# Kernel tuning notes

Hardware: AMD Instinct MI355X
Metric: run time of the kernel (lower is better)

## Reference

```python
import jax, jax.numpy as jnp
import numpy as np

B, N, C = 2, 2048, 1536
H = 8
D = C // H  # 192, must match M's size


def setup_inputs() -> dict:
    key = jax.random.key(0)
    ks = jax.random.split(key, 5)
    x = jax.random.normal(ks[0], (B, N, C), dtype=jnp.float32)
    # nn.Linear(dim, 3*dim, bias=False): weight shape (3C, C)
    W_qkv = jax.random.normal(ks[1], (3 * C, C), dtype=jnp.float32) * (C ** -0.5)
    # nn.Linear(dim, dim) with bias
    W_proj = jax.random.normal(ks[2], (C, C), dtype=jnp.float32) * (C ** -0.5)
    b_proj = jnp.zeros((C,), dtype=jnp.float32)
    scale = jnp.asarray(D ** -0.5, dtype=jnp.float32)  # learned scalar, init head_dim**-0.5
    M = jnp.eye(D, dtype=jnp.float32)  # learned Mahalanobis metric, init identity
    return {"x": x, "W_qkv": W_qkv, "W_proj": W_proj, "b_proj": b_proj,
            "scale": scale, "M": M}


def reference(x, W_qkv, W_proj, b_proj, scale, M):
    Bv, Nv, Cv = x.shape
    qkv = x @ W_qkv.T                                  # [B,N,3C]
    qkv = qkv.reshape(Bv, Nv, 3, H, D).transpose(2, 0, 3, 1, 4)  # [3,B,H,N,D]
    q, k, v = qkv[0], qkv[1], qkv[2]
    q_M = q @ M                                        # [B,H,N,D]
    k_M = k @ M                                        # [B,H,N,D]
    qMq = jnp.sum(q * q_M, axis=-1, keepdims=True)     # [B,H,N,1]
    kMk = jnp.sum(k * k_M, axis=-1, keepdims=True)     # [B,H,N,1]
    kMk = jnp.swapaxes(kMk, -2, -1)                    # [B,H,1,N]
    qMk = jnp.einsum('bhnd,bhmd->bhnm', q_M, k)        # [B,H,N,N]
    dists = qMq + kMk - 2.0 * qMk                      # Mahalanobis quadratic form
    attn = jax.nn.softmax(-dists * scale, axis=-1)     # [B,H,N,N]
    out = jnp.einsum('bhnm,bhmd->bhnd', attn, v)       # [B,H,N,D]
    out = jnp.swapaxes(out, 1, 2).reshape(Bv, Nv, Cv)  # [B,N,C]
    out = out @ W_proj.T + b_proj
    return (out, attn, M)
```

## Files before the change

kernel.cpp:

```cpp
#include <hip/hip_runtime.h>

typedef _Float16 f16;
typedef __attribute__((ext_vector_type(8))) _Float16 f16x8;
typedef __attribute__((ext_vector_type(4))) float f32x4;

#define LOG2E 1.4426950408889634f
#define MFMA16(a, b, c) __builtin_amdgcn_mfma_f32_16x16x32_f16((a), (b), (c), 0, 0, 0)


__device__ __forceinline__ void gl16(const void* g, void* l) {
    __builtin_amdgcn_global_load_lds(
        (const __attribute__((address_space(1))) unsigned int*)g,
        (__attribute__((address_space(3))) unsigned int*)l, 16, 0, 0);
}

__global__ void k_cvt(const float* __restrict__ src, f16* __restrict__ dst, int n4) {
    int i = blockIdx.x * blockDim.x + threadIdx.x;
    if (i >= n4) return;
    float4 v = ((const float4*)src)[i];
    union { f16 h[4]; short4 s4; } u;
    u.h[0] = (f16)v.x; u.h[1] = (f16)v.y; u.h[2] = (f16)v.z; u.h[3] = (f16)v.w;
    ((short4*)dst)[i] = u.s4;
}

__global__ void k_cvtM(const float* __restrict__ M, f16* __restrict__ Mt) {
    int i = blockIdx.x * 256 + threadIdx.x;
    if (i >= 192 * 192) return;
    int d = i / 192, e = i - (i / 192) * 192;
    Mt[d * 192 + e] = (f16)M[e * 192 + d];
}

__global__ __launch_bounds__(256) void k_gemm_qkv(
    const f16* __restrict__ A, const f16* __restrict__ Bw,
    f16* __restrict__ Qh, f16* __restrict__ Kh, f16* __restrict__ Vp)
{
    __shared__ __align__(16) char S[32768];
    const int tid = threadIdx.x, lane = tid & 63, w = tid >> 6;
    const int bid = blockIdx.x;
    const int xcd = bid & 7, cc = bid >> 3;
    const int mb = xcd * 4 + cc / 36, nb = cc - (cc / 36) * 36;
    const int m0 = mb * 128, n0 = nb * 128;
    const int sec = nb >= 24 ? 2 : (nb >= 12 ? 1 : 0);
    const int wm = (w & 1) * 64, wn = (w >> 1) * 64;
    const int L = lane & 15, g = lane >> 4;
    const char* Ab = (const char*)A;
    const char* Bb = (const char*)Bw;

    const char* gA[2]; const char* gB[2]; int ldso[2];
#pragma unroll
    for (int q = 0; q < 2; ++q) {
        int s = w * 128 + q * 64 + lane;
        int swz = ((s & 3) ^ ((s >> 2) & 3)) * 16;
        gA[q] = Ab + (size_t)(m0 + (s >> 2)) * 3072 + swz;
        gB[q] = Bb + (size_t)(n0 + (s >> 2)) * 3072 + swz;
        ldso[q] = w * 2048 + q * 1024;
    }
    const int gx = ((g ^ (L & 3)) << 4);

    f32x4 acc[4][4] = {};
#pragma unroll
    for (int q = 0; q < 2; ++q) {
        gl16(gA[q], S + ldso[q]);
        gl16(gB[q], S + 8192 + ldso[q]);
    }
    int buf = 0;
    for (int kk = 0; kk < 48; ++kk) {
        __syncthreads();
        if (kk < 47) {
            int nb_ = (buf ^ 1) * 16384;
#pragma unroll
            for (int q = 0; q < 2; ++q) {
                gl16(gA[q] + (kk + 1) * 64, S + nb_ + ldso[q]);
                gl16(gB[q] + (kk + 1) * 64, S + nb_ + 8192 + ldso[q]);
            }
        }
        const char* AsB = S + buf * 16384;
        const char* BsB = AsB + 8192;
        f16x8 af[4], bf[4];
#pragma unroll
        for (int i = 0; i < 4; ++i) {
            af[i] = *(const f16x8*)(AsB + (wm + i * 16 + L) * 64 + gx);
            bf[i] = *(const f16x8*)(BsB + (wn + i * 16 + L) * 64 + gx);
        }
        if (sec < 2) {
#pragma unroll
            for (int i = 0; i < 4; ++i)
#pragma unroll
                for (int j = 0; j < 4; ++j)
                    acc[i][j] = MFMA16(bf[j], af[i], acc[i][j]);
        } else {
#pragma unroll
            for (int i = 0; i < 4; ++i)
#pragma unroll
                for (int j = 0; j < 4; ++j)
                    acc[i][j] = MFMA16(af[i], bf[j], acc[i][j]);
        }
        buf ^= 1;
    }

    if (sec == 2) {
#pragma unroll
        for (int i = 0; i < 4; ++i)
#pragma unroll
            for (int j = 0; j < 4; ++j) {
                int rem = n0 + wn + j * 16 + L - 3072;
                int h = rem / 192, d = rem - h * 192;
                int gm = m0 + wm + i * 16 + g * 4;
                int gb = gm >> 11, nn = gm & 2047;
                union { f16 h4[4]; short4 s4; } u;
#pragma unroll
                for (int r = 0; r < 4; ++r) u.h4[r] = (f16)acc[i][j][r];
                int nnp = (nn & ~31) | (((nn >> 2) & 3) << 3) | (((nn >> 4) & 1) << 2) | (nn & 3);
                *(short4*)(Vp + (size_t)((gb * 8 + h) * 192 + d) * 2048 + nnp) = u.s4;
            }
    } else {
        f16* base = sec == 0 ? Qh : Kh;
#pragma unroll
        for (int i = 0; i < 4; ++i) {
            int gm = m0 + wm + i * 16 + L;
            int gb = gm >> 11, nn = gm & 2047;
#pragma unroll
            for (int j = 0; j < 4; ++j) {
                int rem = n0 + wn + j * 16 + g * 4 - sec * 1536;
                int h = rem / 192, d = rem - h * 192;
                union { f16 h4[4]; short4 s4; } u;
#pragma unroll
                for (int r = 0; r < 4; ++r) u.h4[r] = (f16)acc[i][j][r];
                *(short4*)(base + (size_t)((gb * 8 + h) * 2048 + nn) * 192 + d) = u.s4;
            }
        }
    }
}

__global__ __launch_bounds__(256) void k_mgemm(
    const f16* __restrict__ Qh, const f16* __restrict__ Kh,
    const f16* __restrict__ Mt, f16* __restrict__ QMh,
    const float* __restrict__ scale_p, float* __restrict__ qmq, float* __restrict__ kmk)
{
    const int tid = threadIdx.x, lane = tid & 63, w = tid >> 6;
    const int L = lane & 15, g = lane >> 4;
    const int isK = blockIdx.y;
    const f16* src = isK ? Kh : Qh;
    float* rowdot = isK ? kmk : qmq;
    const int row0 = blockIdx.x * 64 + w * 16;
    const int tokrow = row0 + L;
    f16x8 af[6];
#pragma unroll
    for (int ks = 0; ks < 6; ++ks)
        af[ks] = *(const f16x8*)((const char*)src + (size_t)tokrow * 384 + ks * 64 + g * 16);
    f32x4 acc[12] = {};
#pragma unroll
    for (int ct = 0; ct < 12; ++ct)
#pragma unroll
        for (int ks = 0; ks < 6; ++ks) {
            f16x8 bf = *(const f16x8*)((const char*)Mt + (ct * 16 + L) * 384 + ks * 64 + g * 16);
            acc[ct] = MFMA16(bf, af[ks], acc[ct]);
        }
    if (!isK) {
#pragma unroll
        for (int ct = 0; ct < 12; ++ct) {
            union { f16 h4[4]; short4 s4; } u;
#pragma unroll
            for (int r = 0; r < 4; ++r) u.h4[r] = (f16)acc[ct][r];
            *(short4*)(QMh + (size_t)tokrow * 192 + ct * 16 + g * 4) = u.s4;
        }
    }
    float s = 0.f;
#pragma unroll
    for (int ct = 0; ct < 12; ++ct) {
        union { short4 s4; f16 h[4]; } kv;
        kv.s4 = *(const short4*)(src + (size_t)tokrow * 192 + ct * 16 + g * 4);
#pragma unroll
        for (int r = 0; r < 4; ++r) s += acc[ct][r] * (float)kv.h[r];
    }
    s += __shfl_xor(s, 16); s += __shfl_xor(s, 32);
    if (lane < 16) rowdot[row0 + lane] = s * scale_p[0] * LOG2E;
}

__global__ __launch_bounds__(256) void k_attn(
    const f16* __restrict__ QMh, const f16* __restrict__ Kh,
    const f16* __restrict__ Vp, const float* __restrict__ kmk,
    const float* __restrict__ qmq, const float* __restrict__ scale_p,
    float* __restrict__ attn, f16* __restrict__ ctx, float* __restrict__ lrow)
{
    __shared__ __align__(16) char KsB[2][12288];
    __shared__ __align__(16) char VsB[2][15360];
    const int tid = threadIdx.x, lane = tid & 63, w = tid >> 6;
    const int L = lane & 15, g = lane >> 4;
    const int bx = blockIdx.x;
    const int bh = (bx & 7) * 2 + (bx >> 8);
    const int qb = (bx >> 3) & 31;
    const int row0 = qb * 64 + w * 16;
    const float a2 = 2.f * scale_p[0] * LOG2E;

    const char* qbase = (const char*)QMh + (size_t)(bh * 2048 + row0) * 384;
    f16x8 qf[6];
#pragma unroll
    for (int ks = 0; ks < 6; ++ks)
        qf[ks] = *(const f16x8*)(qbase + L * 384 + ks * 64 + g * 16);
    const char* Kb = (const char*)Kh + (size_t)bh * 2048 * 384;
    const char* Vb = (const char*)Vp + (size_t)bh * 192 * 4096;
    const float* kmkrow = kmk + bh * 2048;
    const float Crow = qmq[bh * 2048 + row0 + L];

    int ksrc[3], kdst[3], vsrc[3], vdst[3];
#pragma unroll
    for (int i = 0; i < 3; ++i) {
        int s = tid + 256 * i;
        int r = s / 24, c16 = s - r * 24;
        ksrc[i] = r * 384 + c16 * 16;
        kdst[i] = r * 384 + (((c16 & ~7) | ((c16 & 7) ^ (r & 7))) << 4);
        vsrc[i] = (s >> 2) * 4096 + (s & 3) * 16;
        vdst[i] = (s >> 2) * 80 + (s & 3) * 16;
    }
    int kslot[6];
#pragma unroll
    for (int ks = 0; ks < 6; ++ks) {
        int slot = ks * 4 + g;
        kslot[ks] = (((slot & ~7) | ((slot & 7) ^ (L & 7))) << 4);
    }

    int4 stk[3], stv[3];
#pragma unroll
    for (int i = 0; i < 3; ++i) {
        stk[i] = *(const int4*)(Kb + ksrc[i]);
        stv[i] = *(const int4*)(Vb + vsrc[i]);
    }
    f32x4 cacc[12] = {};
    float lacc = 0.f;
    float m_run = -3.0e38f, sc = 0.f;
    float* arow = attn + (size_t)(bh * 2048 + row0 + L) * 2048;

    for (int c = 0; c < 64; ++c) {
        char* Kl = KsB[c & 1];
        char* Vl = VsB[c & 1];
#pragma unroll
        for (int i = 0; i < 3; ++i) {
            *(int4*)(Kl + kdst[i]) = stk[i];
            *(int4*)(Vl + vdst[i]) = stv[i];
        }
        if (c < 63) {
#pragma unroll
            for (int i = 0; i < 3; ++i) {
                stk[i] = *(const int4*)(Kb + (size_t)(c + 1) * 12288 + ksrc[i]);
                stv[i] = *(const int4*)(Vb + (size_t)(c + 1) * 64 + vsrc[i]);
            }
        }
        __syncthreads();
        f32x4 a0 = {}, a1 = {};
#pragma unroll
        for (int ks = 0; ks < 6; ++ks) {
            f16x8 kf0 = *(const f16x8*)(Kl + L * 384 + kslot[ks]);
            f16x8 kf1 = *(const f16x8*)(Kl + (16 + L) * 384 + kslot[ks]);
            a0 = MFMA16(kf0, qf[ks], a0);
            a1 = MFMA16(kf1, qf[ks], a1);
        }
        float4 km0 = *(const float4*)(kmkrow + c * 32 + g * 4);
        float4 km1 = *(const float4*)(kmkrow + c * 32 + 16 + g * 4);
        float e8[8];
        e8[0] = a2 * a0[0] - km0.x - Crow;
        e8[1] = a2 * a0[1] - km0.y - Crow;
        e8[2] = a2 * a0[2] - km0.z - Crow;
        e8[3] = a2 * a0[3] - km0.w - Crow;
        e8[4] = a2 * a1[0] - km1.x - Crow;
        e8[5] = a2 * a1[1] - km1.y - Crow;
        e8[6] = a2 * a1[2] - km1.z - Crow;
        e8[7] = a2 * a1[3] - km1.w - Crow;
        float mx = fmaxf(fmaxf(fmaxf(e8[0], e8[1]), fmaxf(e8[2], e8[3])),
                         fmaxf(fmaxf(e8[4], e8[5]), fmaxf(e8[6], e8[7])));
        mx = fmaxf(mx, __shfl_xor(mx, 16));
        mx = fmaxf(mx, __shfl_xor(mx, 32));
        if (__any(mx > m_run + 4.f)) {
            float mnew = fmaxf(m_run, mx);
            float fr = __builtin_amdgcn_exp2f(m_run - mnew);
            lacc *= fr;
            float frc[4];
#pragma unroll
            for (int r = 0; r < 4; ++r) frc[r] = __shfl(fr, g * 4 + r);
#pragma unroll
            for (int dt = 0; dt < 12; ++dt)
#pragma unroll
                for (int r = 0; r < 4; ++r) cacc[dt][r] *= frc[r];
            m_run = mnew;
            sc = __builtin_amdgcn_exp2f(-m_run);
        }
        float p[8], ps[8];
#pragma unroll
        for (int j = 0; j < 8; ++j) {
            p[j] = __builtin_amdgcn_exp2f(e8[j]);
            ps[j] = p[j] * sc;
        }
        *(float4*)(arow + c * 32 + g * 4)      = make_float4(p[0], p[1], p[2], p[3]);
        *(float4*)(arow + c * 32 + 16 + g * 4) = make_float4(p[4], p[5], p[6], p[7]);
        lacc += ((ps[0] + ps[1]) + (ps[2] + ps[3])) + ((ps[4] + ps[5]) + (ps[6] + ps[7]));
        f16x8 pa;
        pa[0] = (f16)ps[0]; pa[1] = (f16)ps[1]; pa[2] = (f16)ps[2]; pa[3] = (f16)ps[3];
        pa[4] = (f16)ps[4]; pa[5] = (f16)ps[5]; pa[6] = (f16)ps[6]; pa[7] = (f16)ps[7];
#pragma unroll
        for (int dt = 0; dt < 12; ++dt) {
            f16x8 vf = *(const f16x8*)(Vl + (dt * 16 + L) * 80 + g * 16);
            cacc[dt] = MFMA16(pa, vf, cacc[dt]);
        }
    }
    lacc += __shfl_xor(lacc, 16);
    lacc += __shfl_xor(lacc, 32);
    if (g == 0) lrow[bh * 2048 + row0 + L] = __builtin_amdgcn_exp2f(-m_run) / lacc;
    float linv_r[4];
#pragma unroll
    for (int r = 0; r < 4; ++r) linv_r[r] = 1.f / __shfl(lacc, g * 4 + r);

    __syncthreads();
    char* scr = (char*)KsB + w * 6144;
#pragma unroll
    for (int dt = 0; dt < 12; ++dt)
#pragma unroll
        for (int r = 0; r < 4; ++r)
            *(f16*)(scr + (g * 4 + r) * 384 + (dt * 16 + L) * 2)
                = (f16)(cacc[dt][r] * linv_r[r]);
    const int b = bh >> 3, h = bh & 7;
#pragma unroll
    for (int t = 0; t < 6; ++t) {
        int chunk = t * 64 + lane;
        int tok = chunk / 24, c16 = chunk - tok * 24;
        int4 v = *(const int4*)(scr + tok * 384 + c16 * 16);
        *(int4*)((char*)ctx + ((size_t)(b * 2048 + row0 + tok) * 1536 + h * 192) * 2 + c16 * 16) = v;
    }
}

__global__ __launch_bounds__(256) void k_norm(float* __restrict__ attn,
                                              const float* __restrict__ lrow)
{
    const int row = blockIdx.x * 8 + (threadIdx.x >> 5);
    const int t = threadIdx.x & 31;
    const float f = lrow[row];
    float4* p = (float4*)(attn + (size_t)row * 2048) + t;
#pragma unroll
    for (int i = 0; i < 16; ++i) {
        float4 v = p[(size_t)i * 32];
        v.x *= f; v.y *= f; v.z *= f; v.w *= f;
        p[(size_t)i * 32] = v;
    }
}

__global__ __launch_bounds__(256) void k_proj(
    const f16* __restrict__ A, const f16* __restrict__ Bw,
    const float* __restrict__ bias, float* __restrict__ out)
{
    __shared__ __align__(16) char S[32768];
    const int tid = threadIdx.x, lane = tid & 63, w = tid >> 6;
    const int bid = blockIdx.x;
    const int xcd = bid & 7, cc = bid >> 3;
    const int mb = xcd * 4 + cc / 12, nbk = cc - (cc / 12) * 12;
    const int m0 = mb * 128, n0 = nbk * 128;
    const int wm = (w & 1) * 64, wn = (w >> 1) * 64;
    const int L = lane & 15, g = lane >> 4;
    const char* Ab = (const char*)A;
    const char* Bb = (const char*)Bw;

    const char* gA[2]; const char* gB[2]; int ldso[2];
#pragma unroll
    for (int q = 0; q < 2; ++q) {
        int s = w * 128 + q * 64 + lane;
        int swz = ((s & 3) ^ ((s >> 2) & 3)) * 16;
        gA[q] = Ab + (size_t)(m0 + (s >> 2)) * 3072 + swz;
        gB[q] = Bb + (size_t)(n0 + (s >> 2)) * 3072 + swz;
        ldso[q] = w * 2048 + q * 1024;
    }
    const int gx = ((g ^ (L & 3)) << 4);

    f32x4 acc[4][4] = {};
#pragma unroll
    for (int q = 0; q < 2; ++q) {
        gl16(gA[q], S + ldso[q]);
        gl16(gB[q], S + 8192 + ldso[q]);
    }
    int buf = 0;
    for (int kk = 0; kk < 48; ++kk) {
        __syncthreads();
        if (kk < 47) {
            int nb_ = (buf ^ 1) * 16384;
#pragma unroll
            for (int q = 0; q < 2; ++q) {
                gl16(gA[q] + (kk + 1) * 64, S + nb_ + ldso[q]);
                gl16(gB[q] + (kk + 1) * 64, S + nb_ + 8192 + ldso[q]);
            }
        }
        const char* AsB = S + buf * 16384;
        const char* BsB = AsB + 8192;
        f16x8 af[4], bf[4];
#pragma unroll
        for (int i = 0; i < 4; ++i) {
            af[i] = *(const f16x8*)(AsB + (wm + i * 16 + L) * 64 + gx);
            bf[i] = *(const f16x8*)(BsB + (wn + i * 16 + L) * 64 + gx);
        }
#pragma unroll
        for (int i = 0; i < 4; ++i)
#pragma unroll
            for (int j = 0; j < 4; ++j)
                acc[i][j] = MFMA16(bf[j], af[i], acc[i][j]);
        buf ^= 1;
    }
#pragma unroll
    for (int i = 0; i < 4; ++i) {
        int token = m0 + wm + i * 16 + L;
#pragma unroll
        for (int j = 0; j < 4; ++j) {
            int gnb = n0 + wn + j * 16 + g * 4;
            float4 bv = *(const float4*)(bias + gnb);
            float4 v = make_float4(acc[i][j][0] + bv.x, acc[i][j][1] + bv.y,
                                   acc[i][j][2] + bv.z, acc[i][j][3] + bv.w);
            *(float4*)(out + (size_t)token * 1536 + gnb) = v;
        }
    }
}

extern "C" void kernel_launch(void* const* d_in, const int* in_sizes, int n_in,
                              void* d_out, int out_size, void* d_ws, size_t ws_size,
                              hipStream_t stream)
{
    const float* x     = (const float*)d_in[0];
    const float* Wqkv  = (const float*)d_in[1];
    const float* Wproj = (const float*)d_in[2];
    const float* bproj = (const float*)d_in[3];
    const float* scale = (const float*)d_in[4];
    const float* M     = (const float*)d_in[5];
    float* out  = (float*)d_out;
    float* attn = out + 6291456;

    char* p = (char*)d_ws;
    f16* x_h     = (f16*)p;  p += 12582912;
    f16* Wqkv_h  = (f16*)p;  p += 14155776;
    f16* Wproj_h = (f16*)p;  p += 4718592;
    f16* Mt_h    = (f16*)p;  p += 73728;
    f16* Qh      = (f16*)p;  p += 12582912;
    f16* Kh      = (f16*)p;  p += 12582912;
    f16* Vp      = (f16*)p;  p += 12582912;
    f16* QMh     = (f16*)p;  p += 12582912;
    float* qmq   = (float*)p; p += 131072;
    float* kmk   = (float*)p; p += 131072;
    float* lrow  = (float*)p; p += 131072;
    f16* ctx     = (f16*)p;  p += 12582912;

    k_cvt<<<6144, 256, 0, stream>>>(x, x_h, 1572864);
    k_cvt<<<6912, 256, 0, stream>>>(Wqkv, Wqkv_h, 1769472);
    k_cvt<<<2304, 256, 0, stream>>>(Wproj, Wproj_h, 589824);
    k_cvtM<<<144, 256, 0, stream>>>(M, Mt_h);
    k_gemm_qkv<<<1152, 256, 0, stream>>>(x_h, Wqkv_h, Qh, Kh, Vp);
    k_mgemm<<<dim3(512, 2), 256, 0, stream>>>(Qh, Kh, Mt_h, QMh, scale, qmq, kmk);
    k_attn<<<512, 256, 0, stream>>>(QMh, Kh, Vp, kmk, qmq, scale, attn, ctx, lrow);
    k_norm<<<4096, 256, 0, stream>>>(attn, lrow);
    k_proj<<<384, 256, 0, stream>>>(ctx, Wproj_h, bproj, out);
    hipMemcpyAsync(out + 73400320, M, 36864 * 4, hipMemcpyDeviceToDevice, stream);
}
```

Before: 447.8 us.

## Precompute softmax row stats, split attention over key halves, drop normalize pass

Adds a stats kernel that computes the row max and log-sum per query row with a QK-only pass. The attention kernel then writes already-normalized probabilities directly, so the separate read-modify-write normalization of the attention matrix is gone. Attention is split into two key halves to double the block count, with fp32 partial outputs summed by a new combine kernel. The three fp32-to-fp16 conversion launches are merged into one. In exchange, QK^T is recomputed, a large fp32 partial buffer is written and read, and the V tile is single-buffered behind an extra barrier.

```diff
diff --git a/kernel.cpp b/kernel.cpp
--- a/kernel.cpp
+++ b/kernel.cpp
@@ -14,13 +14,18 @@
         (__attribute__((address_space(3))) unsigned int*)l, 16, 0, 0);
 }
 
-__global__ void k_cvt(const float* __restrict__ src, f16* __restrict__ dst, int n4) {
-    int i = blockIdx.x * blockDim.x + threadIdx.x;
-    if (i >= n4) return;
-    float4 v = ((const float4*)src)[i];
+__global__ void k_cvt_all(const float* __restrict__ x, const float* __restrict__ wq,
+                          const float* __restrict__ wp, f16* __restrict__ xh,
+                          f16* __restrict__ wqh, f16* __restrict__ wph) {
+    int i = blockIdx.x * 256 + threadIdx.x;
+    const float4* s; short4* d; int off;
+    if (i < 1572864) { s = (const float4*)x; d = (short4*)xh; off = i; }
+    else if (i < 3342336) { s = (const float4*)wq; d = (short4*)wqh; off = i - 1572864; }
+    else { s = (const float4*)wp; d = (short4*)wph; off = i - 3342336; }
+    float4 v = s[off];
     union { f16 h[4]; short4 s4; } u;
     u.h[0] = (f16)v.x; u.h[1] = (f16)v.y; u.h[2] = (f16)v.z; u.h[3] = (f16)v.w;
-    ((short4*)dst)[i] = u.s4;
+    d[off] = u.s4;
 }
 
 __global__ void k_cvtM(const float* __restrict__ M, f16* __restrict__ Mt) {
@@ -177,14 +182,12 @@
     if (lane < 16) rowdot[row0 + lane] = s * scale_p[0] * LOG2E;
 }
 
-__global__ __launch_bounds__(256) void k_attn(
+__global__ __launch_bounds__(256) void k_stats(
     const f16* __restrict__ QMh, const f16* __restrict__ Kh,
-    const f16* __restrict__ Vp, const float* __restrict__ kmk,
-    const float* __restrict__ qmq, const float* __restrict__ scale_p,
-    float* __restrict__ attn, f16* __restrict__ ctx, float* __restrict__ lrow)
+    const float* __restrict__ kmk, const float* __restrict__ qmq,
+    const float* __restrict__ scale_p, float* __restrict__ moff)
 {
     __shared__ __align__(16) char KsB[2][12288];
-    __shared__ __align__(16) char VsB[2][15360];
     const int tid = threadIdx.x, lane = tid & 63, w = tid >> 6;
     const int L = lane & 15, g = lane >> 4;
     const int bx = blockIdx.x;
@@ -199,19 +202,16 @@
     for (int ks = 0; ks < 6; ++ks)
         qf[ks] = *(const f16x8*)(qbase + L * 384 + ks * 64 + g * 16);
     const char* Kb = (const char*)Kh + (size_t)bh * 2048 * 384;
-    const char* Vb = (const char*)Vp + (size_t)bh * 192 * 4096;
     const float* kmkrow = kmk + bh * 2048;
     const float Crow = qmq[bh * 2048 + row0 + L];
 
-    int ksrc[3], kdst[3], vsrc[3], vdst[3];
+    int ksrc[3], kdst[3];
 #pragma unroll
     for (int i = 0; i < 3; ++i) {
         int s = tid + 256 * i;
         int r = s / 24, c16 = s - r * 24;
         ksrc[i] = r * 384 + c16 * 16;
         kdst[i] = r * 384 + (((c16 & ~7) | ((c16 & 7) ^ (r & 7))) << 4);
-        vsrc[i] = (s >> 2) * 4096 + (s & 3) * 16;
-        vdst[i] = (s >> 2) * 80 + (s & 3) * 16;
     }
     int kslot[6];
 #pragma unroll
@@ -219,32 +219,19 @@
         int slot = ks * 4 + g;
         kslot[ks] = (((slot & ~7) | ((slot & 7) ^ (L & 7))) << 4);
     }
-
-    int4 stk[3], stv[3];
-#pragma unroll
-    for (int i = 0; i < 3; ++i) {
-        stk[i] = *(const int4*)(Kb + ksrc[i]);
-        stv[i] = *(const int4*)(Vb + vsrc[i]);
-    }
-    f32x4 cacc[12] = {};
-    float lacc = 0.f;
-    float m_run = -3.0e38f, sc = 0.f;
-    float* arow = attn + (size_t)(bh * 2048 + row0 + L) * 2048;
-
+    int4 stk[3];
+#pragma unroll
+    for (int i = 0; i < 3; ++i) stk[i] = *(const int4*)(Kb + ksrc[i]);
+
+    float m_run = -3.0e38f, l_run = 0.f;
     for (int c = 0; c < 64; ++c) {
         char* Kl = KsB[c & 1];
-        char* Vl = VsB[c & 1];
-#pragma unroll
-        for (int i = 0; i < 3; ++i) {
-            *(int4*)(Kl + kdst[i]) = stk[i];
-            *(int4*)(Vl + vdst[i]) = stv[i];
-        }
+#pragma unroll
+        for (int i = 0; i < 3; ++i) *(int4*)(Kl + kdst[i]) = stk[i];
         if (c < 63) {
 #pragma unroll
-            for (int i = 0; i < 3; ++i) {
+            for (int i = 0; i < 3; ++i)
                 stk[i] = *(const int4*)(Kb + (size_t)(c + 1) * 12288 + ksrc[i]);
-                stv[i] = *(const int4*)(Vb + (size_t)(c + 1) * 64 + vsrc[i]);
-            }
         }
         __syncthreads();
         f32x4 a0 = {}, a1 = {};
@@ -270,76 +257,146 @@
                          fmaxf(fmaxf(e8[4], e8[5]), fmaxf(e8[6], e8[7])));
         mx = fmaxf(mx, __shfl_xor(mx, 16));
         mx = fmaxf(mx, __shfl_xor(mx, 32));
-        if (__any(mx > m_run + 4.f)) {
-            float mnew = fmaxf(m_run, mx);
-            float fr = __builtin_amdgcn_exp2f(m_run - mnew);
-            lacc *= fr;
-            float frc[4];
-#pragma unroll
-            for (int r = 0; r < 4; ++r) frc[r] = __shfl(fr, g * 4 + r);
-#pragma unroll
-            for (int dt = 0; dt < 12; ++dt)
-#pragma unroll
-                for (int r = 0; r < 4; ++r) cacc[dt][r] *= frc[r];
-            m_run = mnew;
-            sc = __builtin_amdgcn_exp2f(-m_run);
-        }
-        float p[8], ps[8];
-#pragma unroll
-        for (int j = 0; j < 8; ++j) {
-            p[j] = __builtin_amdgcn_exp2f(e8[j]);
-            ps[j] = p[j] * sc;
-        }
+        float mn = fmaxf(m_run, mx);
+        float sum = 0.f;
+#pragma unroll
+        for (int j = 0; j < 8; ++j) sum += __builtin_amdgcn_exp2f(e8[j] - mn);
+        l_run = l_run * __builtin_amdgcn_exp2f(m_run - mn) + sum;
+        m_run = mn;
+    }
+    l_run += __shfl_xor(l_run, 16);
+    l_run += __shfl_xor(l_run, 32);
+    if (g == 0) moff[bh * 2048 + row0 + L] = m_run + __log2f(l_run);
+}
+
+__global__ __launch_bounds__(256, 4) void k_attn(
+    const f16* __restrict__ QMh, const f16* __restrict__ Kh,
+    const f16* __restrict__ Vp, const float* __restrict__ kmk,
+    const float* __restrict__ qmq, const float* __restrict__ scale_p,
+    const float* __restrict__ moff,
+    float* __restrict__ attn, float* __restrict__ pacc)
+{
+    __shared__ __align__(16) char KsB[2][12288];
+    __shared__ __align__(16) char VsB[15360];
+    const int tid = threadIdx.x, lane = tid & 63, w = tid >> 6;
+    const int L = lane & 15, g = lane >> 4;
+    const int bx = blockIdx.x;
+    const int xcd = bx & 7, cc = bx >> 3;
+    const int bh = xcd * 2 + (cc >> 6);
+    const int qb = (cc >> 1) & 31;
+    const int kh = cc & 1;
+    const int c0 = kh * 32;
+    const int row0 = qb * 64 + w * 16;
+    const float a2 = 2.f * scale_p[0] * LOG2E;
+
+    const char* qbase = (const char*)QMh + (size_t)(bh * 2048 + row0) * 384;
+    f16x8 qf[6];
+#pragma unroll
+    for (int ks = 0; ks < 6; ++ks)
+        qf[ks] = *(const f16x8*)(qbase + L * 384 + ks * 64 + g * 16);
+    const char* Kb = (const char*)Kh + (size_t)bh * 2048 * 384;
+    const char* Vb = (const char*)Vp + (size_t)bh * 192 * 4096;
+    const float* kmkrow = kmk + bh * 2048;
+    const float Crow = qmq[bh * 2048 + row0 + L];
+    const float mo = moff[bh * 2048 + row0 + L];
+
+    int ksrc[3], kdst[3], vsrc[3], vdst[3];
+#pragma unroll
+    for (int i = 0; i < 3; ++i) {
+        int s = tid + 256 * i;
+        int r = s / 24, c16 = s - r * 24;
+        ksrc[i] = r * 384 + c16 * 16;
+        kdst[i] = r * 384 + (((c16 & ~7) | ((c16 & 7) ^ (r & 7))) << 4);
+        vsrc[i] = (s >> 2) * 4096 + (s & 3) * 16;
+        vdst[i] = (s >> 2) * 80 + (s & 3) * 16;
+    }
+    int kslot[6];
+#pragma unroll
+    for (int ks = 0; ks < 6; ++ks) {
+        int slot = ks * 4 + g;
+        kslot[ks] = (((slot & ~7) | ((slot & 7) ^ (L & 7))) << 4);
+    }
+
+    int4 stk[3], stv[3];
+#pragma unroll
+    for (int i = 0; i < 3; ++i) {
+        stk[i] = *(const int4*)(Kb + (size_t)c0 * 12288 + ksrc[i]);
+        stv[i] = *(const int4*)(Vb + (size_t)c0 * 64 + vsrc[i]);
+    }
+    f32x4 cacc[12] = {};
+    float* arow = attn + (size_t)(bh * 2048 + row0 + L) * 2048;
+
+    for (int cl = 0; cl < 32; ++cl) {
+        const int c = c0 + cl;
+        char* Kl = KsB[cl & 1];
+#pragma unroll
+        for (int i = 0; i < 3; ++i) *(int4*)(Kl + kdst[i]) = stk[i];
+        __syncthreads();
+#pragma unroll
+        for (int i = 0; i < 3; ++i) *(int4*)(VsB + vdst[i]) = stv[i];
+        __syncthreads();
+        if (cl < 31) {
+#pragma unroll
+            for (int i = 0; i < 3; ++i) {
+                stk[i] = *(const int4*)(Kb + (size_t)(c + 1) * 12288 + ksrc[i]);
+                stv[i] = *(const int4*)(Vb + (size_t)(c + 1) * 64 + vsrc[i]);
+            }
+        }
+        f32x4 a0 = {}, a1 = {};
+#pragma unroll
+        for (int ks = 0; ks < 6; ++ks) {
+            f16x8 kf0 = *(const f16x8*)(Kl + L * 384 + kslot[ks]);
+            f16x8 kf1 = *(const f16x8*)(Kl + (16 + L) * 384 + kslot[ks]);
+            a0 = MFMA16(kf0, qf[ks], a0);
+            a1 = MFMA16(kf1, qf[ks], a1);
+        }
+        float4 km0 = *(const float4*)(kmkrow + c * 32 + g * 4);
+        float4 km1 = *(const float4*)(kmkrow + c * 32 + 16 + g * 4);
+        float p[8];
+        p[0] = __builtin_amdgcn_exp2f(a2 * a0[0] - km0.x - Crow - mo);
+        p[1] = __builtin_amdgcn_exp2f(a2 * a0[1] - km0.y - Crow - mo);
+        p[2] = __builtin_amdgcn_exp2f(a2 * a0[2] - km0.z - Crow - mo);
+        p[3] = __builtin_amdgcn_exp2f(a2 * a0[3] - km0.w - Crow - mo);
+        p[4] = __builtin_amdgcn_exp2f(a2 * a1[0] - km1.x - Crow - mo);
+        p[5] = __builtin_amdgcn_exp2f(a2 * a1[1] - km1.y - Crow - mo);
+        p[6] = __builtin_amdgcn_exp2f(a2 * a1[2] - km1.z - Crow - mo);
+        p[7] = __builtin_amdgcn_exp2f(a2 * a1[3] - km1.w - Crow - mo);
         *(float4*)(arow + c * 32 + g * 4)      = make_float4(p[0], p[1], p[2], p[3]);
         *(float4*)(arow + c * 32 + 16 + g * 4) = make_float4(p[4], p[5], p[6], p[7]);
-        lacc += ((ps[0] + ps[1]) + (ps[2] + ps[3])) + ((ps[4] + ps[5]) + (ps[6] + ps[7]));
         f16x8 pa;
-        pa[0] = (f16)ps[0]; pa[1] = (f16)ps[1]; pa[2] = (f16)ps[2]; pa[3] = (f16)ps[3];
-        pa[4] = (f16)ps[4]; pa[5] = (f16)ps[5]; pa[6] = (f16)ps[6]; pa[7] = (f16)ps[7];
+        pa[0] = (f16)p[0]; pa[1] = (f16)p[1]; pa[2] = (f16)p[2]; pa[3] = (f16)p[3];
+        pa[4] = (f16)p[4]; pa[5] = (f16)p[5]; pa[6] = (f16)p[6]; pa[7] = (f16)p[7];
 #pragma unroll
         for (int dt = 0; dt < 12; ++dt) {
-            f16x8 vf = *(const f16x8*)(Vl + (dt * 16 + L) * 80 + g * 16);
+            f16x8 vf = *(const f16x8*)(VsB + (dt * 16 + L) * 80 + g * 16);
             cacc[dt] = MFMA16(pa, vf, cacc[dt]);
         }
     }
-    lacc += __shfl_xor(lacc, 16);
-    lacc += __shfl_xor(lacc, 32);
-    if (g == 0) lrow[bh * 2048 + row0 + L] = __builtin_amdgcn_exp2f(-m_run) / lacc;
-    float linv_r[4];
-#pragma unroll
-    for (int r = 0; r < 4; ++r) linv_r[r] = 1.f / __shfl(lacc, g * 4 + r);
-
-    __syncthreads();
-    char* scr = (char*)KsB + w * 6144;
 #pragma unroll
     for (int dt = 0; dt < 12; ++dt)
 #pragma unroll
         for (int r = 0; r < 4; ++r)
-            *(f16*)(scr + (g * 4 + r) * 384 + (dt * 16 + L) * 2)
-                = (f16)(cacc[dt][r] * linv_r[r]);
-    const int b = bh >> 3, h = bh & 7;
-#pragma unroll
-    for (int t = 0; t < 6; ++t) {
-        int chunk = t * 64 + lane;
-        int tok = chunk / 24, c16 = chunk - tok * 24;
-        int4 v = *(const int4*)(scr + tok * 384 + c16 * 16);
-        *(int4*)((char*)ctx + ((size_t)(b * 2048 + row0 + tok) * 1536 + h * 192) * 2 + c16 * 16) = v;
-    }
-}
-
-__global__ __launch_bounds__(256) void k_norm(float* __restrict__ attn,
-                                              const float* __restrict__ lrow)
-{
-    const int row = blockIdx.x * 8 + (threadIdx.x >> 5);
-    const int t = threadIdx.x & 31;
-    const float f = lrow[row];
-    float4* p = (float4*)(attn + (size_t)row * 2048) + t;
-#pragma unroll
-    for (int i = 0; i < 16; ++i) {
-        float4 v = p[(size_t)i * 32];
-        v.x *= f; v.y *= f; v.z *= f; v.w *= f;
-        p[(size_t)i * 32] = v;
-    }
+            pacc[((size_t)kh * 32768 + bh * 2048 + row0 + g * 4 + r) * 192 + dt * 16 + L]
+                = cacc[dt][r];
+}
+
+__global__ __launch_bounds__(256) void k_comb(const float* __restrict__ pacc,
+                                              f16* __restrict__ ctx)
+{
+    int idx = blockIdx.x * 256 + threadIdx.x;
+    int row = idx / 24;
+    int d = (idx - row * 24) * 8;
+    const float* p0 = pacc + (size_t)row * 192 + d;
+    const float* p1 = p0 + (size_t)32768 * 192;
+    float4 a0 = *(const float4*)p0, a1 = *(const float4*)(p0 + 4);
+    float4 b0 = *(const float4*)p1, b1 = *(const float4*)(p1 + 4);
+    union { f16 h[8]; int4 v; } u;
+    u.h[0] = (f16)(a0.x + b0.x); u.h[1] = (f16)(a0.y + b0.y);
+    u.h[2] = (f16)(a0.z + b0.z); u.h[3] = (f16)(a0.w + b0.w);
+    u.h[4] = (f16)(a1.x + b1.x); u.h[5] = (f16)(a1.y + b1.y);
+    u.h[6] = (f16)(a1.z + b1.z); u.h[7] = (f16)(a1.w + b1.w);
+    int bh = row >> 11, nr = row & 2047;
+    *(int4*)(ctx + (size_t)((bh >> 3) * 2048 + nr) * 1536 + (bh & 7) * 192 + d) = u.v;
 }
 
 __global__ __launch_bounds__(256) void k_proj(
@@ -438,17 +495,17 @@
     f16* QMh     = (f16*)p;  p += 12582912;
     float* qmq   = (float*)p; p += 131072;
     float* kmk   = (float*)p; p += 131072;
-    float* lrow  = (float*)p; p += 131072;
+    float* moff  = (float*)p; p += 131072;
+    float* pacc  = (float*)p; p += 50331648;
     f16* ctx     = (f16*)p;  p += 12582912;
 
-    k_cvt<<<6144, 256, 0, stream>>>(x, x_h, 1572864);
-    k_cvt<<<6912, 256, 0, stream>>>(Wqkv, Wqkv_h, 1769472);
-    k_cvt<<<2304, 256, 0, stream>>>(Wproj, Wproj_h, 589824);
+    k_cvt_all<<<15360, 256, 0, stream>>>(x, Wqkv, Wproj, x_h, Wqkv_h, Wproj_h);
     k_cvtM<<<144, 256, 0, stream>>>(M, Mt_h);
     k_gemm_qkv<<<1152, 256, 0, stream>>>(x_h, Wqkv_h, Qh, Kh, Vp);
     k_mgemm<<<dim3(512, 2), 256, 0, stream>>>(Qh, Kh, Mt_h, QMh, scale, qmq, kmk);
-    k_attn<<<512, 256, 0, stream>>>(QMh, Kh, Vp, kmk, qmq, scale, attn, ctx, lrow);
-    k_norm<<<4096, 256, 0, stream>>>(attn, lrow);
+    k_stats<<<512, 256, 0, stream>>>(QMh, Kh, kmk, qmq, scale, moff);
+    k_attn<<<1024, 256, 0, stream>>>(QMh, Kh, Vp, kmk, qmq, scale, moff, attn, pacc);
+    k_comb<<<3072, 256, 0, stream>>>(pacc, ctx);
     k_proj<<<384, 256, 0, stream>>>(ctx, Wproj_h, bproj, out);
     hipMemcpyAsync(out + 73400320, M, 36864 * 4, hipMemcpyDeviceToDevice, stream);
 }
```

Measured after the change: 686.0 us. 1.53x slower.

## Fuse attention-row normalization into attn kernel and merge fp32-to-fp16 conversions

Applied to the files above, without the earlier changes.

Drops the separate k_norm pass. Each wave now rescales its own attention rows right after the online softmax finishes, reading back the rows it just wrote (likely still in cache) and storing them with nontemporal writes. This is meant to cut a full extra kernel's global read/write sweep over the 128MB attention matrix. The three input conversion launches are also merged into one kernel to save launch overhead. In exchange, each attn block does more serial memory work at its tail, and the reread may miss in L2.

```diff
diff --git a/kernel.cpp b/kernel.cpp
--- a/kernel.cpp
+++ b/kernel.cpp
@@ -14,13 +14,18 @@
         (__attribute__((address_space(3))) unsigned int*)l, 16, 0, 0);
 }
 
-__global__ void k_cvt(const float* __restrict__ src, f16* __restrict__ dst, int n4) {
-    int i = blockIdx.x * blockDim.x + threadIdx.x;
-    if (i >= n4) return;
-    float4 v = ((const float4*)src)[i];
+__global__ void k_cvt_all(const float* __restrict__ x, const float* __restrict__ wq,
+                          const float* __restrict__ wp, f16* __restrict__ xh,
+                          f16* __restrict__ wqh, f16* __restrict__ wph) {
+    int i = blockIdx.x * 256 + threadIdx.x;
+    const float4* s; short4* d; int off;
+    if (i < 1572864) { s = (const float4*)x; d = (short4*)xh; off = i; }
+    else if (i < 3342336) { s = (const float4*)wq; d = (short4*)wqh; off = i - 1572864; }
+    else { s = (const float4*)wp; d = (short4*)wph; off = i - 3342336; }
+    float4 v = s[off];
     union { f16 h[4]; short4 s4; } u;
     u.h[0] = (f16)v.x; u.h[1] = (f16)v.y; u.h[2] = (f16)v.z; u.h[3] = (f16)v.w;
-    ((short4*)dst)[i] = u.s4;
+    d[off] = u.s4;
 }
 
 __global__ void k_cvtM(const float* __restrict__ M, f16* __restrict__ Mt) {
@@ -181,7 +186,7 @@
     const f16* __restrict__ QMh, const f16* __restrict__ Kh,
     const f16* __restrict__ Vp, const float* __restrict__ kmk,
     const float* __restrict__ qmq, const float* __restrict__ scale_p,
-    float* __restrict__ attn, f16* __restrict__ ctx, float* __restrict__ lrow)
+    float* __restrict__ attn, f16* __restrict__ ctx)
 {
     __shared__ __align__(16) char KsB[2][12288];
     __shared__ __align__(16) char VsB[2][15360];
@@ -304,10 +309,20 @@
     }
     lacc += __shfl_xor(lacc, 16);
     lacc += __shfl_xor(lacc, 32);
-    if (g == 0) lrow[bh * 2048 + row0 + L] = __builtin_amdgcn_exp2f(-m_run) / lacc;
+    const float fnorm = __builtin_amdgcn_exp2f(-m_run) / lacc;
     float linv_r[4];
 #pragma unroll
     for (int r = 0; r < 4; ++r) linv_r[r] = 1.f / __shfl(lacc, g * 4 + r);
+
+#pragma unroll 4
+    for (int c = 0; c < 64; ++c) {
+        f32x4 v0 = *(const f32x4*)(arow + c * 32 + g * 4);
+        f32x4 v1 = *(const f32x4*)(arow + c * 32 + 16 + g * 4);
+        v0 *= fnorm;
+        v1 *= fnorm;
+        __builtin_nontemporal_store(v0, (f32x4*)(arow + c * 32 + g * 4));
+        __builtin_nontemporal_store(v1, (f32x4*)(arow + c * 32 + 16 + g * 4));
+    }
 
     __syncthreads();
     char* scr = (char*)KsB + w * 6144;
@@ -324,21 +339,6 @@
         int tok = chunk / 24, c16 = chunk - tok * 24;
         int4 v = *(const int4*)(scr + tok * 384 + c16 * 16);
         *(int4*)((char*)ctx + ((size_t)(b * 2048 + row0 + tok) * 1536 + h * 192) * 2 + c16 * 16) = v;
-    }
-}
-
-__global__ __launch_bounds__(256) void k_norm(float* __restrict__ attn,
-                                              const float* __restrict__ lrow)
-{
-    const int row = blockIdx.x * 8 + (threadIdx.x >> 5);
-    const int t = threadIdx.x & 31;
-    const float f = lrow[row];
-    float4* p = (float4*)(attn + (size_t)row * 2048) + t;
-#pragma unroll
-    for (int i = 0; i < 16; ++i) {
-        float4 v = p[(size_t)i * 32];
-        v.x *= f; v.y *= f; v.z *= f; v.w *= f;
-        p[(size_t)i * 32] = v;
     }
 }
 
@@ -438,17 +438,13 @@
     f16* QMh     = (f16*)p;  p += 12582912;
     float* qmq   = (float*)p; p += 131072;
     float* kmk   = (float*)p; p += 131072;
-    float* lrow  = (float*)p; p += 131072;
     f16* ctx     = (f16*)p;  p += 12582912;
 
-    k_cvt<<<6144, 256, 0, stream>>>(x, x_h, 1572864);
-    k_cvt<<<6912, 256, 0, stream>>>(Wqkv, Wqkv_h, 1769472);
-    k_cvt<<<2304, 256, 0, stream>>>(Wproj, Wproj_h, 589824);
+    k_cvt_all<<<15360, 256, 0, stream>>>(x, Wqkv, Wproj, x_h, Wqkv_h, Wproj_h);
     k_cvtM<<<144, 256, 0, stream>>>(M, Mt_h);
     k_gemm_qkv<<<1152, 256, 0, stream>>>(x_h, Wqkv_h, Qh, Kh, Vp);
     k_mgemm<<<dim3(512, 2), 256, 0, stream>>>(Qh, Kh, Mt_h, QMh, scale, qmq, kmk);
-    k_attn<<<512, 256, 0, stream>>>(QMh, Kh, Vp, kmk, qmq, scale, attn, ctx, lrow);
-    k_norm<<<4096, 256, 0, stream>>>(attn, lrow);
+    k_attn<<<512, 256, 0, stream>>>(QMh, Kh, Vp, kmk, qmq, scale, attn, ctx);
     k_proj<<<384, 256, 0, stream>>>(ctx, Wproj_h, bproj, out);
     hipMemcpyAsync(out + 73400320, M, 36864 * 4, hipMemcpyDeviceToDevice, stream);
 }
```

After: 448.4 us. About the same (+0.1%).
